# Performance work log

Hardware: AMD Instinct MI355X
Metric: run time of the kernel (lower is better)

## Reference

```python
import jax, jax.numpy as jnp
import numpy as np

B, L, D, H, DK, DV = 2, 2048, 512, 8, 64, 64
EPS = 1e-6


def setup_inputs() -> dict:
    key = jax.random.key(0)
    ks = jax.random.split(key, 19)
    n = lambda k, s: jax.random.normal(k, s, dtype=jnp.float32)
    inp = {
        "q_r": n(ks[0], (B, L, D)), "q_i": n(ks[1], (B, L, D)),
        "k_r": n(ks[2], (B, L, D)), "k_i": n(ks[3], (B, L, D)),
        "v_r": n(ks[4], (B, L, D)), "v_i": n(ks[5], (B, L, D)),
        "wq_r": n(ks[6], (D, H * DK)) * 0.02, "wq_i": n(ks[7], (D, H * DK)) * 0.02,
        "wk_r": n(ks[8], (D, H * DK)) * 0.02, "wk_i": n(ks[9], (D, H * DK)) * 0.02,
        "wv_r": n(ks[10], (D, H * DV)) * 0.02, "wv_i": n(ks[11], (D, H * DV)) * 0.02,
        "wo_r": n(ks[12], (H * DV, D)) * 0.02, "wo_i": n(ks[13], (H * DV, D)) * 0.02,
        "ln_wr": n(ks[14], (D,)), "ln_wi": n(ks[15], (D,)),
        "ln_br": n(ks[16], (D,)), "ln_bi": n(ks[17], (D,)),
        "mask": jax.random.randint(ks[18], (B, L, L), 0, 2).astype(jnp.int32),
    }
    return inp


def _clinear(xr, xi, wr, wi):
    # complex matmul (xr + i xi) @ (wr + i wi)
    return xr @ wr - xi @ wi, xi @ wr + xr @ wi


def _complex_layernorm(r, i, wr, wi, br, bi, eps=EPS):
    axes = (1, 2)  # normalize over all non-batch dims of [B, L, D]
    r = r - r.mean(axis=axes, keepdims=True)
    i = i - i.mean(axis=axes, keepdims=True)
    Crr = (r * r).mean(axis=axes, keepdims=True) + eps
    Cii = (i * i).mean(axis=axes, keepdims=True) + eps
    Cri = (r * i).mean(axis=axes, keepdims=True)
    s = jnp.sqrt(Crr * Cii - Cri * Cri)
    t = jnp.sqrt(Crr + Cii + 2.0 * s)
    inv_st = 1.0 / (s * t)
    Rrr = (Cii + s) * inv_st
    Rii = (Crr + s) * inv_st
    Rri = -Cri * inv_st
    nr = Rrr * r + Rri * i
    ni = Rii * i + Rri * r
    # affine: complex multiply by (wr + i wi), then add complex bias
    out_r = nr * wr - ni * wi + br
    out_i = nr * wi + ni * wr + bi
    return out_r, out_i


def reference(q_r, q_i, k_r, k_i, v_r, v_i,
              wq_r, wq_i, wk_r, wk_i, wv_r, wv_i, wo_r, wo_i,
              ln_wr, ln_wi, ln_br, ln_bi, mask):
    res_r, res_i = q_r, q_i
    qr, qi = _clinear(q_r, q_i, wq_r, wq_i)
    kr, ki = _clinear(k_r, k_i, wk_r, wk_i)
    vr, vi = _clinear(v_r, v_i, wv_r, wv_i)
    # [B, L, H*Dk] -> [B, H, L, Dk]
    tohead = lambda x, d: x.reshape(B, L, H, d).transpose(0, 2, 1, 3)
    qr, qi = tohead(qr, DK), tohead(qi, DK)
    kr, ki = tohead(kr, DK), tohead(ki, DK)
    vr, vi = tohead(vr, DV), tohead(vi, DV)
    temp = jnp.float32(DK) ** 0.5
    qr, qi = qr / temp, qi / temp
    # complex scores (q @ conj(k)^T): re + i*im
    sr = jnp.einsum('bhqd,bhkd->bhqk', qr, kr) + jnp.einsum('bhqd,bhkd->bhqk', qi, ki)
    si = jnp.einsum('bhqd,bhkd->bhqk', qi, kr) - jnp.einsum('bhqd,bhkd->bhqk', qr, ki)
    a = jnp.sqrt(sr * sr + si * si)  # abs of complex scores
    a = jnp.where(mask[:, None, :, :] == 0, jnp.float32(-1e9), a)
    attn = jax.nn.softmax(a, axis=-1)  # real-valued attention weights
    out_r = jnp.einsum('bhqk,bhkd->bhqd', attn, vr)
    out_i = jnp.einsum('bhqk,bhkd->bhqd', attn, vi)
    # [B, H, L, Dv] -> [B, L, H*Dv]
    out_r = out_r.transpose(0, 2, 1, 3).reshape(B, L, H * DV)
    out_i = out_i.transpose(0, 2, 1, 3).reshape(B, L, H * DV)
    out_r, out_i = _clinear(out_r, out_i, wo_r, wo_i)
    out_r = out_r + res_r
    out_i = out_i + res_i
    out_r, out_i = _complex_layernorm(out_r, out_i, ln_wr, ln_wi, ln_br, ln_bi)
    return out_r, out_i, attn
```

## Files before the change

### kernel.cpp

```cpp
#include <hip/hip_runtime.h>

typedef unsigned short u16;
typedef unsigned int u32;
typedef unsigned long long u64;


typedef __attribute__((ext_vector_type(8))) short bf16x8;
typedef __attribute__((ext_vector_type(4))) float f32x4;
typedef __attribute__((ext_vector_type(4))) u32 u32x4;

__device__ __forceinline__ u16 f2bf(float f) {
  u32 x = __float_as_uint(f);
  return (u16)((x + 0x7FFFu + ((x >> 16) & 1u)) >> 16);
}
__device__ __forceinline__ u32 pk2(float a, float b) {
  return (u32)f2bf(a) | ((u32)f2bf(b) << 16);
}
__device__ __forceinline__ bf16x8 negv(bf16x8 v) {
  u32x4 x = __builtin_bit_cast(u32x4, v);
  x ^= 0x80008000u;
  return __builtin_bit_cast(bf16x8, x);
}

__global__ __launch_bounds__(256) void prep(
    const float* __restrict__ qr, const float* __restrict__ qi,
    const float* __restrict__ kr, const float* __restrict__ ki,
    const float* __restrict__ vr, const float* __restrict__ vi,
    const float* __restrict__ wqr, const float* __restrict__ wqi,
    const float* __restrict__ wkr, const float* __restrict__ wki,
    const float* __restrict__ wvr, const float* __restrict__ wvi,
    const float* __restrict__ wor, const float* __restrict__ woi,
    const int* __restrict__ mask,
    u16* __restrict__ A, u16* __restrict__ Btb, u64* __restrict__ mb,
    float* __restrict__ stats) {
  __shared__ float tile[64][65];
  int bid = blockIdx.x;
  int t = threadIdx.x;
  if (bid < 32768) {
    int tid = bid * 256 + t;
    u64 bal = __ballot(mask[tid] != 0);
    if ((t & 63) == 0) mb[tid >> 6] = bal;
    return;
  }
  bid -= 32768;
  if (bid < 6144) {
    int z = bid >> 11;
    int bx = bid & 2047;
    const float* r  = (z == 0) ? qr : (z == 1) ? kr : vr;
    const float* im = (z == 0) ? qi : (z == 1) ? ki : vi;
    int c = bx * 256 + t;
    int m = c >> 7;
    int ck = (c & 127) * 8;
    const float* s = (ck < 512) ? (r + (size_t)m * 512 + ck)
                                : (im + (size_t)m * 512 + (ck - 512));
    float4 a = ((const float4*)s)[0];
    float4 b = ((const float4*)s)[1];
    uint4 o;
    o.x = pk2(a.x, a.y); o.y = pk2(a.z, a.w);
    o.z = pk2(b.x, b.y); o.w = pk2(b.z, b.w);
    ((uint4*)(A + (size_t)z * 4194304))[c] = o;
    return;
  }
  bid -= 6144;
  if (bid < 1024) {
    int z = bid >> 8;
    int bx = bid & 255;
    const float* wr = (z==0)?wqr:(z==1)?wkr:(z==2)?wvr:wor;
    const float* wi = (z==0)?wqi:(z==1)?wki:(z==2)?wvi:woi;
    u16* Bt = Btb + (size_t)z * 1048576;
    int n0 = (bx >> 4) * 64;
    int k0 = (bx & 15) * 64;
    bool nlow = (n0 < 512), klow = (k0 < 512);
    const float* src = nlow ? (klow ? wr : wi) : (klow ? wi : wr);
    float sgn = (nlow && !klow) ? -1.0f : 1.0f;
    int col0 = nlow ? n0 : n0 - 512;
    int kr0 = klow ? k0 : k0 - 512;
    {
      int rr = t >> 2, cc = (t & 3) * 16;
      const float4* s = (const float4*)(src + (size_t)(kr0 + rr) * 512 + col0 + cc);
#pragma unroll
      for (int j = 0; j < 4; ++j) {
        float4 v = s[j];
        tile[rr][cc + j*4 + 0] = v.x; tile[rr][cc + j*4 + 1] = v.y;
        tile[rr][cc + j*4 + 2] = v.z; tile[rr][cc + j*4 + 3] = v.w;
      }
    }
    __syncthreads();
    {
      int nn = t >> 2, kc = (t & 3) * 16;
      u32 w[8];
#pragma unroll
      for (int j = 0; j < 8; ++j)
        w[j] = pk2(sgn * tile[kc + 2*j][nn], sgn * tile[kc + 2*j + 1][nn]);
      uint4* d = (uint4*)(Bt + (size_t)(n0 + nn) * 1024 + k0 + kc);
      d[0] = make_uint4(w[0], w[1], w[2], w[3]);
      d[1] = make_uint4(w[4], w[5], w[6], w[7]);
    }
    return;
  }
  if (t < 16) stats[t] = 0.0f;
}

__global__ __launch_bounds__(256) void pack_vt(const u16* __restrict__ Cvm,
                                               u16* __restrict__ vt) {
  int z = blockIdx.y;
  int b = z >> 3, h = z & 7;
  int lt = blockIdx.x >> 1, ct = blockIdx.x & 1;
  int l0 = lt * 64, c0 = ct * 64;
  int n0 = (ct == 0) ? (h * 64) : (512 + h * 64);
  __shared__ u16 tile[64][80];
  int t = threadIdx.x;
  {
    int lr = t >> 2, cc = (t & 3) * 16;
    const uint4* s = (const uint4*)(Cvm + ((size_t)(b * 2048 + l0 + lr)) * 1024 + n0 + cc);
    uint4 v0 = s[0], v1 = s[1];
    *(uint4*)&tile[lr][cc] = v0;
    *(uint4*)&tile[lr][cc + 8] = v1;
  }
  __syncthreads();
  {
    int cr = t >> 2, lc = (t & 3) * 16;
    u32 w[8];
#pragma unroll
    for (int j = 0; j < 8; ++j)
      w[j] = (u32)tile[lc + 2*j][cr] | ((u32)tile[lc + 2*j + 1][cr] << 16);
    uint4* d = (uint4*)(vt + ((size_t)z * 128 + c0 + cr) * 2048 + l0 + lc);
    d[0] = make_uint4(w[0], w[1], w[2], w[3]);
    d[1] = make_uint4(w[4], w[5], w[6], w[7]);
  }
}

__device__ __forceinline__ void glds128(const u16* __restrict__ g, int ld,
                                        u16* lds, int t) {
  int lane = t & 63, w = t >> 6;
  int sub = lane >> 3;
  int cs = (lane & 7) ^ sub;
#pragma unroll
  for (int p = 0; p < 4; ++p) {
    int r = p * 32 + w * 8 + sub;
    const u16* ga = g + (size_t)r * ld + cs * 8;
    u16* la = lds + (size_t)(p * 32 + w * 8) * 64;
    __builtin_amdgcn_global_load_lds(
        (const __attribute__((address_space(1))) void*)ga,
        (__attribute__((address_space(3))) void*)la, 16, 0, 0);
  }
}
__device__ __forceinline__ void glds64(const u16* __restrict__ g, int ld,
                                       u16* lds, int t) {
  int lane = t & 63, w = t >> 6;
  int sub = lane >> 3;
  int cs = (lane & 7) ^ sub;
#pragma unroll
  for (int p = 0; p < 2; ++p) {
    int r = p * 32 + w * 8 + sub;
    const u16* ga = g + (size_t)r * ld + cs * 8;
    u16* la = lds + (size_t)(p * 32 + w * 8) * 64;
    __builtin_amdgcn_global_load_lds(
        (const __attribute__((address_space(1))) void*)ga,
        (__attribute__((address_space(3))) void*)la, 16, 0, 0);
  }
}

__global__ __launch_bounds__(256) void gemm_proj(const u16* __restrict__ Abase,
                                                 const u16* __restrict__ Btbase,
                                                 u16* __restrict__ Cbase) {
  __shared__ u16 lA[128 * 64], lB[128 * 64];
  int t = threadIdx.x, lane = t & 63, wid = t >> 6;
  int c15 = lane & 15, g = lane >> 4, l7 = lane & 7;
  int z = blockIdx.z;
  const u16* A  = Abase  + (size_t)z * 4194304;
  const u16* Bt = Btbase + (size_t)z * 1048576;
  u16* C = Cbase + (size_t)z * 4194304;
  int brow = blockIdx.y * 128, bcol = blockIdx.x * 128;
  float scale = (z == 0) ? 0.125f : 1.0f;
  int sw0 = ((g ^ l7) << 3), sw1 = (((4 | g) ^ l7) << 3);
  int wr0 = (wid >> 1) * 64 + c15, wc0 = (wid & 1) * 64 + c15;
  const u16 *pA0 = lA + wr0 * 64 + sw0, *pA1 = lA + wr0 * 64 + sw1;
  const u16 *pB0 = lB + wc0 * 64 + sw0, *pB1 = lB + wc0 * 64 + sw1;
  f32x4 zero = {0.f, 0.f, 0.f, 0.f};
  f32x4 acc[4][4];
#pragma unroll
  for (int mi = 0; mi < 4; ++mi)
#pragma unroll
    for (int ni = 0; ni < 4; ++ni) acc[mi][ni] = zero;
  for (int kt = 0; kt < 1024; kt += 64) {
    glds128(A + (size_t)brow * 1024 + kt, 1024, lA, t);
    glds128(Bt + (size_t)bcol * 1024 + kt, 1024, lB, t);
    __syncthreads();
#pragma unroll
    for (int ks = 0; ks < 2; ++ks) {
      const u16* pa = ks ? pA1 : pA0;
      const u16* pb = ks ? pB1 : pB0;
      bf16x8 fa[4], fb[4];
#pragma unroll
      for (int i2 = 0; i2 < 4; ++i2) {
        fa[i2] = *(const bf16x8*)(pa + i2 * 1024);
        fb[i2] = *(const bf16x8*)(pb + i2 * 1024);
      }
#pragma unroll
      for (int mi = 0; mi < 4; ++mi)
#pragma unroll
        for (int ni = 0; ni < 4; ++ni)
          acc[mi][ni] = __builtin_amdgcn_mfma_f32_16x16x32_bf16(
              fa[mi], fb[ni], acc[mi][ni], 0, 0, 0);
    }
    __syncthreads();
  }
  int wrb = (wid >> 1) * 64, wcb = (wid & 1) * 64;
  int rj = g * 4, cj = c15;
#pragma unroll
  for (int mi = 0; mi < 4; ++mi)
#pragma unroll
    for (int ni = 0; ni < 4; ++ni)
#pragma unroll
      for (int j = 0; j < 4; ++j)
        C[(size_t)(brow + wrb + mi * 16 + rj + j) * 1024 +
          (bcol + wcb + ni * 16 + cj)] = f2bf(acc[mi][ni][j] * scale);
}

__global__ __launch_bounds__(256, 3) void fused_p1(
    const u16* __restrict__ Cq, const u16* __restrict__ Ck,
    const u16* __restrict__ vt, const u64* __restrict__ mb,
    float* __restrict__ invbuf, u16* __restrict__ Ao) {
  __shared__ u16 lKr[64 * 64], lKi[64 * 64], lV[128 * 64], lP[64 * 64];
  int t = threadIdx.x, lane = t & 63, w = t >> 6;
  int c15 = lane & 15, g = lane >> 4, l7 = lane & 7;
  int f = blockIdx.x + (int)gridDim.x * blockIdx.y;
  int wk = (f & 7) * 64 + (f >> 3);
  int strip = wk & 31, z = wk >> 5;
  int b = z >> 3, h = z & 7;
  int q0 = strip * 64;
  int arow = w * 16 + c15;
  int rbase = w * 16 + (g << 2);

  const u16* Qrow = Cq + ((size_t)(b * 2048 + q0 + arow)) * 1024 + h * 64;
  bf16x8 q0r = *(const bf16x8*)(Qrow + g * 8);
  bf16x8 q1r = *(const bf16x8*)(Qrow + 32 + g * 8);
  bf16x8 q0i = *(const bf16x8*)(Qrow + 512 + g * 8);
  bf16x8 q1i = *(const bf16x8*)(Qrow + 544 + g * 8);
  bf16x8 nq0r = negv(q0r), nq1r = negv(q1r);

  int sw0 = ((g ^ l7) << 3), sw1 = (((4 | g) ^ l7) << 3);
  const u16 *pKr0 = lKr + c15 * 64 + sw0, *pKr1 = lKr + c15 * 64 + sw1;
  const u16 *pKi0 = lKi + c15 * 64 + sw0, *pKi1 = lKi + c15 * 64 + sw1;
  const u16 *pV0 = lV + c15 * 64 + sw0, *pV1 = lV + c15 * 64 + sw1;
  const u16 *pP0 = lP + arow * 64 + sw0, *pP1 = lP + arow * 64 + sw1;

  size_t mbase = ((size_t)(b * 2048 + q0 + rbase)) * 32;
  float s[4] = {0.f, 0.f, 0.f, 0.f};
  f32x4 zero = {0.f, 0.f, 0.f, 0.f};
  f32x4 o[8];
#pragma unroll
  for (int ni = 0; ni < 8; ++ni) o[ni] = zero;

  const u16* Kb = Ck + ((size_t)(b * 2048)) * 1024 + h * 64;
  const u16* Vb = vt + (size_t)z * 262144;

  for (int tl = 0; tl < 32; ++tl) {
    int l0 = tl * 64;
    if (tl) __syncthreads();
    glds64(Kb + (size_t)l0 * 1024, 1024, lKr, t);
    glds64(Kb + (size_t)l0 * 1024 + 512, 1024, lKi, t);
    glds128(Vb + l0, 2048, lV, t);
    __syncthreads();
    f32x4 sr[4], si[4];
#pragma unroll
    for (int ni = 0; ni < 4; ++ni) { sr[ni] = zero; si[ni] = zero; }
#pragma unroll
    for (int ni = 0; ni < 4; ++ni) {
      bf16x8 g0 = *(const bf16x8*)(pKr0 + ni * 1024);
      bf16x8 g1 = *(const bf16x8*)(pKi0 + ni * 1024);
      sr[ni] = __builtin_amdgcn_mfma_f32_16x16x32_bf16(q0r, g0, sr[ni], 0, 0, 0);
      sr[ni] = __builtin_amdgcn_mfma_f32_16x16x32_bf16(q0i, g1, sr[ni], 0, 0, 0);
      si[ni] = __builtin_amdgcn_mfma_f32_16x16x32_bf16(q0i, g0, si[ni], 0, 0, 0);
      si[ni] = __builtin_amdgcn_mfma_f32_16x16x32_bf16(nq0r, g1, si[ni], 0, 0, 0);
      bf16x8 h0 = *(const bf16x8*)(pKr1 + ni * 1024);
      bf16x8 h1 = *(const bf16x8*)(pKi1 + ni * 1024);
      sr[ni] = __builtin_amdgcn_mfma_f32_16x16x32_bf16(q1r, h0, sr[ni], 0, 0, 0);
      sr[ni] = __builtin_amdgcn_mfma_f32_16x16x32_bf16(q1i, h1, sr[ni], 0, 0, 0);
      si[ni] = __builtin_amdgcn_mfma_f32_16x16x32_bf16(q1i, h0, si[ni], 0, 0, 0);
      si[ni] = __builtin_amdgcn_mfma_f32_16x16x32_bf16(nq1r, h1, si[ni], 0, 0, 0);
    }
    u64 wm[4];
#pragma unroll
    for (int j = 0; j < 4; ++j) wm[j] = mb[mbase + (size_t)j * 32 + tl];
#pragma unroll
    for (int ni = 0; ni < 4; ++ni) {
      int cbit = ni * 16 + c15;
      int pchi = ni * 2 + (c15 >> 3);
#pragma unroll
      for (int j = 0; j < 4; ++j) {
        float n = sr[ni][j] * sr[ni][j] + si[ni][j] * si[ni][j];
        float p = __expf(__builtin_amdgcn_sqrtf(n));
        p = ((wm[j] >> cbit) & 1ull) ? p : 0.0f;
        s[j] += p;
        lP[(rbase + j) * 64 + ((pchi ^ (((g & 1) << 2) + j)) << 3) + l7] = f2bf(p);
      }
    }
    {
      bf16x8 fa0 = *(const bf16x8*)pP0;
      bf16x8 fa1 = *(const bf16x8*)pP1;
#pragma unroll
      for (int ni = 0; ni < 8; ++ni) {
        bf16x8 fb0 = *(const bf16x8*)(pV0 + ni * 1024);
        bf16x8 fb1 = *(const bf16x8*)(pV1 + ni * 1024);
        o[ni] = __builtin_amdgcn_mfma_f32_16x16x32_bf16(fa0, fb0, o[ni], 0, 0, 0);
        o[ni] = __builtin_amdgcn_mfma_f32_16x16x32_bf16(fa1, fb1, o[ni], 0, 0, 0);
      }
    }
  }
  float inv[4];
#pragma unroll
  for (int j = 0; j < 4; ++j) {
    float sj = s[j];
#pragma unroll
    for (int off = 1; off < 16; off <<= 1) sj += __shfl_xor(sj, off);
    inv[j] = 1.0f / sj;
  }
  if (c15 == 0) {
#pragma unroll
    for (int j = 0; j < 4; ++j)
      invbuf[z * 2048 + q0 + rbase + j] = inv[j];
  }
#pragma unroll
  for (int ni = 0; ni < 8; ++ni) {
    int c = ni * 16 + c15;
    int nout = (c < 64) ? (h * 64 + c) : (512 + h * 64 + (c - 64));
#pragma unroll
    for (int j = 0; j < 4; ++j)
      Ao[((size_t)(b * 2048 + q0 + rbase + j)) * 1024 + nout] =
          f2bf(o[ni][j] * inv[j]);
  }
}

__global__ __launch_bounds__(256, 3) void attn_p2(
    const u16* __restrict__ Cq, const u16* __restrict__ Ck,
    const u64* __restrict__ mb, const float* __restrict__ invbuf,
    float* __restrict__ attn) {
  __shared__ u16 lKr[64 * 64], lKi[64 * 64];
  int t = threadIdx.x, lane = t & 63, w = t >> 6;
  int c15 = lane & 15, g = lane >> 4, l7 = lane & 7;
  int f = blockIdx.x + (int)gridDim.x * blockIdx.y;
  int wk = (f & 7) * 256 + (f >> 3);
  int z = wk >> 7;
  int rem = wk & 127;
  int strip = rem >> 2, kc = rem & 3;
  int b = z >> 3, h = z & 7;
  int q0 = strip * 64;
  int arow = w * 16 + c15;
  int rbase = w * 16 + (g << 2);

  const u16* Qrow = Cq + ((size_t)(b * 2048 + q0 + arow)) * 1024 + h * 64;
  bf16x8 q0r = *(const bf16x8*)(Qrow + g * 8);
  bf16x8 q1r = *(const bf16x8*)(Qrow + 32 + g * 8);
  bf16x8 q0i = *(const bf16x8*)(Qrow + 512 + g * 8);
  bf16x8 q1i = *(const bf16x8*)(Qrow + 544 + g * 8);
  bf16x8 nq0r = negv(q0r), nq1r = negv(q1r);

  int sw0 = ((g ^ l7) << 3), sw1 = (((4 | g) ^ l7) << 3);
  const u16 *pKr0 = lKr + c15 * 64 + sw0, *pKr1 = lKr + c15 * 64 + sw1;
  const u16 *pKi0 = lKi + c15 * 64 + sw0, *pKi1 = lKi + c15 * 64 + sw1;

  size_t mbase = ((size_t)(b * 2048 + q0 + rbase)) * 32;
  float inv[4];
#pragma unroll
  for (int j = 0; j < 4; ++j) inv[j] = invbuf[z * 2048 + q0 + rbase + j];
  f32x4 zero = {0.f, 0.f, 0.f, 0.f};
  const u16* Kb = Ck + ((size_t)(b * 2048)) * 1024 + h * 64;
  float* arow_out = attn + ((size_t)z * 2048 + q0 + rbase) * 2048 + c15;

  for (int tt2 = 0; tt2 < 8; ++tt2) {
    int tl = kc * 8 + tt2;
    int l0 = tl * 64;
    if (tt2) __syncthreads();
    glds64(Kb + (size_t)l0 * 1024, 1024, lKr, t);
    glds64(Kb + (size_t)l0 * 1024 + 512, 1024, lKi, t);
    __syncthreads();
    f32x4 sr[4], si[4];
#pragma unroll
    for (int ni = 0; ni < 4; ++ni) { sr[ni] = zero; si[ni] = zero; }
#pragma unroll
    for (int ni = 0; ni < 4; ++ni) {
      bf16x8 g0 = *(const bf16x8*)(pKr0 + ni * 1024);
      bf16x8 g1 = *(const bf16x8*)(pKi0 + ni * 1024);
      sr[ni] = __builtin_amdgcn_mfma_f32_16x16x32_bf16(q0r, g0, sr[ni], 0, 0, 0);
      sr[ni] = __builtin_amdgcn_mfma_f32_16x16x32_bf16(q0i, g1, sr[ni], 0, 0, 0);
      si[ni] = __builtin_amdgcn_mfma_f32_16x16x32_bf16(q0i, g0, si[ni], 0, 0, 0);
      si[ni] = __builtin_amdgcn_mfma_f32_16x16x32_bf16(nq0r, g1, si[ni], 0, 0, 0);
      bf16x8 h0 = *(const bf16x8*)(pKr1 + ni * 1024);
      bf16x8 h1 = *(const bf16x8*)(pKi1 + ni * 1024);
      sr[ni] = __builtin_amdgcn_mfma_f32_16x16x32_bf16(q1r, h0, sr[ni], 0, 0, 0);
      sr[ni] = __builtin_amdgcn_mfma_f32_16x16x32_bf16(q1i, h1, sr[ni], 0, 0, 0);
      si[ni] = __builtin_amdgcn_mfma_f32_16x16x32_bf16(q1i, h0, si[ni], 0, 0, 0);
      si[ni] = __builtin_amdgcn_mfma_f32_16x16x32_bf16(nq1r, h1, si[ni], 0, 0, 0);
    }
    u64 wm[4];
#pragma unroll
    for (int j = 0; j < 4; ++j) wm[j] = mb[mbase + (size_t)j * 32 + tl];
    float* outp = arow_out + l0;
#pragma unroll
    for (int ni = 0; ni < 4; ++ni) {
      int cbit = ni * 16 + c15;
#pragma unroll
      for (int j = 0; j < 4; ++j) {
        float n = sr[ni][j] * sr[ni][j] + si[ni][j] * si[ni][j];
        float p = __expf(__builtin_amdgcn_sqrtf(n)) * inv[j];
        p = ((wm[j] >> cbit) & 1ull) ? p : 0.0f;
        outp[(size_t)j * 2048 + ni * 16] = p;
      }
    }
  }
}

__global__ __launch_bounds__(256) void gemm_oproj(
    const u16* __restrict__ A, const u16* __restrict__ Bt,
    const float* __restrict__ resR, const float* __restrict__ resI,
    float* __restrict__ outR, float* __restrict__ outI) {
  __shared__ u16 lA[128 * 64], lB[128 * 64];
  int t = threadIdx.x, lane = t & 63, wid = t >> 6;
  int c15 = lane & 15, g = lane >> 4, l7 = lane & 7;
  int brow = blockIdx.y * 128, bcol = blockIdx.x * 128;
  int sw0 = ((g ^ l7) << 3), sw1 = (((4 | g) ^ l7) << 3);
  int wr0 = (wid >> 1) * 64 + c15, wc0 = (wid & 1) * 64 + c15;
  const u16 *pA0 = lA + wr0 * 64 + sw0, *pA1 = lA + wr0 * 64 + sw1;
  const u16 *pB0 = lB + wc0 * 64 + sw0, *pB1 = lB + wc0 * 64 + sw1;
  f32x4 zero = {0.f, 0.f, 0.f, 0.f};
  f32x4 acc[4][4];
#pragma unroll
  for (int mi = 0; mi < 4; ++mi)
#pragma unroll
    for (int ni = 0; ni < 4; ++ni) acc[mi][ni] = zero;
  for (int kt = 0; kt < 1024; kt += 64) {
    glds128(A + (size_t)brow * 1024 + kt, 1024, lA, t);
    glds128(Bt + (size_t)bcol * 1024 + kt, 1024, lB, t);
    __syncthreads();
#pragma unroll
    for (int ks = 0; ks < 2; ++ks) {
      const u16* pa = ks ? pA1 : pA0;
      const u16* pb = ks ? pB1 : pB0;
      bf16x8 fa[4], fb[4];
#pragma unroll
      for (int i2 = 0; i2 < 4; ++i2) {
        fa[i2] = *(const bf16x8*)(pa + i2 * 1024);
        fb[i2] = *(const bf16x8*)(pb + i2 * 1024);
      }
#pragma unroll
      for (int mi = 0; mi < 4; ++mi)
#pragma unroll
        for (int ni = 0; ni < 4; ++ni)
          acc[mi][ni] = __builtin_amdgcn_mfma_f32_16x16x32_bf16(
              fa[mi], fb[ni], acc[mi][ni], 0, 0, 0);
    }
    __syncthreads();
  }
  int wrb = (wid >> 1) * 64, wcb = (wid & 1) * 64;
  int rj = g * 4, cj = c15;
#pragma unroll
  for (int mi = 0; mi < 4; ++mi)
#pragma unroll
    for (int ni = 0; ni < 4; ++ni)
#pragma unroll
      for (int j = 0; j < 4; ++j) {
        int row = brow + wrb + mi * 16 + rj + j;
        int col = bcol + wcb + ni * 16 + cj;
        float v = acc[mi][ni][j];
        if (col < 512)
          outR[(size_t)row * 512 + col] = v + resR[(size_t)row * 512 + col];
        else {
          int c2 = col - 512;
          outI[(size_t)row * 512 + c2] = v + resI[(size_t)row * 512 + c2];
        }
      }
}

__global__ __launch_bounds__(256) void ln_reduce(const float* __restrict__ outR,
                                                 const float* __restrict__ outI,
                                                 float* __restrict__ stats) {
  int b = blockIdx.y;
  int t = threadIdx.x;
  size_t base = (size_t)b * 1048576 + (size_t)blockIdx.x * 2048;
  float s0 = 0.f, s1 = 0.f, s2 = 0.f, s3 = 0.f, s4 = 0.f;
#pragma unroll
  for (int p = 0; p < 8; ++p) {
    size_t e = base + p * 256 + t;
    float r = outR[e], i = outI[e];
    s0 += r; s1 += i; s2 += r * r; s3 += i * i; s4 += r * i;
  }
#pragma unroll
  for (int off = 32; off; off >>= 1) {
    s0 += __shfl_xor(s0, off); s1 += __shfl_xor(s1, off);
    s2 += __shfl_xor(s2, off); s3 += __shfl_xor(s3, off);
    s4 += __shfl_xor(s4, off);
  }
  __shared__ float red[4][5];
  if ((t & 63) == 0) {
    int w = t >> 6;
    red[w][0] = s0; red[w][1] = s1; red[w][2] = s2; red[w][3] = s3; red[w][4] = s4;
  }
  __syncthreads();
  if (t == 0) {
    float a0 = red[0][0] + red[1][0] + red[2][0] + red[3][0];
    float a1 = red[0][1] + red[1][1] + red[2][1] + red[3][1];
    float a2 = red[0][2] + red[1][2] + red[2][2] + red[3][2];
    float a3 = red[0][3] + red[1][3] + red[2][3] + red[3][3];
    float a4 = red[0][4] + red[1][4] + red[2][4] + red[3][4];
    atomicAdd(&stats[b * 8 + 0], a0);
    atomicAdd(&stats[b * 8 + 1], a1);
    atomicAdd(&stats[b * 8 + 2], a2);
    atomicAdd(&stats[b * 8 + 3], a3);
    atomicAdd(&stats[b * 8 + 4], a4);
  }
}

__global__ __launch_bounds__(256) void ln_apply(
    float* __restrict__ outR, float* __restrict__ outI,
    const float* __restrict__ stats,
    const float* __restrict__ lnwr, const float* __restrict__ lnwi,
    const float* __restrict__ lnbr, const float* __restrict__ lnbi) {
  int b = blockIdx.y;
  const float* st = stats + b * 8;
  float iN = 1.0f / 1048576.0f;
  float mr = st[0] * iN, mi = st[1] * iN;
  float Crr = st[2] * iN - mr * mr + 1e-6f;
  float Cii = st[3] * iN - mi * mi + 1e-6f;
  float Cri = st[4] * iN - mr * mi;
  float s = sqrtf(fmaxf(Crr * Cii - Cri * Cri, 0.f));
  float tt = sqrtf(Crr + Cii + 2.f * s);
  float inv = 1.0f / (s * tt);
  float Rrr = (Cii + s) * inv, Rii = (Crr + s) * inv, Rri = -Cri * inv;
  size_t e = ((size_t)blockIdx.x * 256 + threadIdx.x) * 4;
  size_t idx = (size_t)b * 1048576 + e;
  int d = (int)(e & 511);
  float4 r4 = *(float4*)(outR + idx);
  float4 i4 = *(float4*)(outI + idx);
  float4 wr = *(const float4*)(lnwr + d);
  float4 wi = *(const float4*)(lnwi + d);
  float4 br = *(const float4*)(lnbr + d);
  float4 bi = *(const float4*)(lnbi + d);
  float4 orr, oii;
#pragma unroll
  for (int j = 0; j < 4; ++j) {
    float r = ((&r4.x)[j]) - mr;
    float i = ((&i4.x)[j]) - mi;
    float nr = Rrr * r + Rri * i;
    float ni = Rii * i + Rri * r;
    (&orr.x)[j] = nr * (&wr.x)[j] - ni * (&wi.x)[j] + (&br.x)[j];
    (&oii.x)[j] = nr * (&wi.x)[j] + ni * (&wr.x)[j] + (&bi.x)[j];
  }
  *(float4*)(outR + idx) = orr;
  *(float4*)(outI + idx) = oii;
}

extern "C" void kernel_launch(void* const* d_in, const int* in_sizes, int n_in,
                              void* d_out, int out_size, void* d_ws, size_t ws_size,
                              hipStream_t stream) {
  const float* q_r = (const float*)d_in[0];
  const float* q_i = (const float*)d_in[1];
  const float* k_r = (const float*)d_in[2];
  const float* k_i = (const float*)d_in[3];
  const float* v_r = (const float*)d_in[4];
  const float* v_i = (const float*)d_in[5];
  const float* wq_r = (const float*)d_in[6];
  const float* wq_i = (const float*)d_in[7];
  const float* wk_r = (const float*)d_in[8];
  const float* wk_i = (const float*)d_in[9];
  const float* wv_r = (const float*)d_in[10];
  const float* wv_i = (const float*)d_in[11];
  const float* wo_r = (const float*)d_in[12];
  const float* wo_i = (const float*)d_in[13];
  const float* ln_wr = (const float*)d_in[14];
  const float* ln_wi = (const float*)d_in[15];
  const float* ln_br = (const float*)d_in[16];
  const float* ln_bi = (const float*)d_in[17];
  const int* mask = (const int*)d_in[18];

  float* outR = (float*)d_out;
  float* outI = outR + 2097152;
  float* attn = outR + 4194304;

  char* ws = (char*)d_ws;
  u16* Aq = (u16*)ws;
  u16* Bt = (u16*)(ws + 25165824);
  u16* Cq = (u16*)(ws + 33554432);
  u16* Ck = Cq + 4194304;
  u16* Cv = Cq + 8388608;
  u16* vt = Aq;
  u16* Ao = (u16*)(ws + 58720256);
  u64* mb = (u64*)(ws + 67108864);
  float* stats = (float*)(ws + 69206016);
  float* invbuf = (float*)(ws + 69207040);

  prep<<<dim3(32768 + 6144 + 1024 + 1), 256, 0, stream>>>(
      q_r, q_i, k_r, k_i, v_r, v_i, wq_r, wq_i, wk_r, wk_i, wv_r, wv_i,
      wo_r, wo_i, mask, Aq, Bt, mb, stats);
  gemm_proj<<<dim3(8, 32, 3), 256, 0, stream>>>(Aq, Bt, Cq);
  pack_vt<<<dim3(64, 16), 256, 0, stream>>>(Cv, vt);
  fused_p1<<<dim3(32, 16), 256, 0, stream>>>(Cq, Ck, vt, mb, invbuf, Ao);
  attn_p2<<<dim3(128, 16), 256, 0, stream>>>(Cq, Ck, mb, invbuf, attn);
  gemm_oproj<<<dim3(8, 32), 256, 0, stream>>>(Ao, Bt + 3145728, q_r, q_i, outR, outI);
  ln_reduce<<<dim3(512, 2), 256, 0, stream>>>(outR, outI, stats);
  ln_apply<<<dim3(1024, 2), 256, 0, stream>>>(outR, outI, stats, ln_wr, ln_wi,
                                              ln_br, ln_bi);
}
```

Baseline: 338.1 us.

## Halve attention block threads, give each wave two 16-row query tiles

The fused attention and attn-probability kernels now launch 128 threads (2 waves) per 64-row strip instead of 4. Each wave handles 32 query rows, so every K and V fragment read from LDS feeds two tiles' worth of MFMAs. LDS load helpers are rewritten to fill the same tiles with fewer threads. This cuts LDS read traffic per MFMA but doubles register use and halves waves per block, which lowers latency hiding and occupancy.

```diff
diff --git a/kernel.cpp b/kernel.cpp
--- a/kernel.cpp
+++ b/kernel.cpp
@@ -145,16 +145,31 @@
         (__attribute__((address_space(3))) void*)la, 16, 0, 0);
   }
 }
-__device__ __forceinline__ void glds64(const u16* __restrict__ g, int ld,
-                                       u16* lds, int t) {
+__device__ __forceinline__ void glds64h(const u16* __restrict__ g, int ld,
+                                        u16* lds, int t) {
   int lane = t & 63, w = t >> 6;
   int sub = lane >> 3;
   int cs = (lane & 7) ^ sub;
 #pragma unroll
-  for (int p = 0; p < 2; ++p) {
-    int r = p * 32 + w * 8 + sub;
+  for (int p = 0; p < 4; ++p) {
+    int r = p * 16 + w * 8 + sub;
     const u16* ga = g + (size_t)r * ld + cs * 8;
-    u16* la = lds + (size_t)(p * 32 + w * 8) * 64;
+    u16* la = lds + (size_t)(p * 16 + w * 8) * 64;
+    __builtin_amdgcn_global_load_lds(
+        (const __attribute__((address_space(1))) void*)ga,
+        (__attribute__((address_space(3))) void*)la, 16, 0, 0);
+  }
+}
+__device__ __forceinline__ void glds128h(const u16* __restrict__ g, int ld,
+                                         u16* lds, int t) {
+  int lane = t & 63, w = t >> 6;
+  int sub = lane >> 3;
+  int cs = (lane & 7) ^ sub;
+#pragma unroll
+  for (int p = 0; p < 8; ++p) {
+    int r = p * 16 + w * 8 + sub;
+    const u16* ga = g + (size_t)r * ld + cs * 8;
+    u16* la = lds + (size_t)(p * 16 + w * 8) * 64;
     __builtin_amdgcn_global_load_lds(
         (const __attribute__((address_space(1))) void*)ga,
         (__attribute__((address_space(3))) void*)la, 16, 0, 0);
@@ -218,7 +233,7 @@
           (bcol + wcb + ni * 16 + cj)] = f2bf(acc[mi][ni][j] * scale);
 }
 
-__global__ __launch_bounds__(256, 3) void fused_p1(
+__global__ __launch_bounds__(128) void fused_p1(
     const u16* __restrict__ Cq, const u16* __restrict__ Ck,
     const u16* __restrict__ vt, const u64* __restrict__ mb,
     float* __restrict__ invbuf, u16* __restrict__ Ao) {
@@ -230,28 +245,38 @@
   int strip = wk & 31, z = wk >> 5;
   int b = z >> 3, h = z & 7;
   int q0 = strip * 64;
-  int arow = w * 16 + c15;
-  int rbase = w * 16 + (g << 2);
-
-  const u16* Qrow = Cq + ((size_t)(b * 2048 + q0 + arow)) * 1024 + h * 64;
-  bf16x8 q0r = *(const bf16x8*)(Qrow + g * 8);
-  bf16x8 q1r = *(const bf16x8*)(Qrow + 32 + g * 8);
-  bf16x8 q0i = *(const bf16x8*)(Qrow + 512 + g * 8);
-  bf16x8 q1i = *(const bf16x8*)(Qrow + 544 + g * 8);
-  bf16x8 nq0r = negv(q0r), nq1r = negv(q1r);
+  int arow = w * 32 + c15;
+  int rbase = w * 32 + (g << 2);
+
+  bf16x8 q0r[2], q1r[2], q0i[2], q1i[2], nq0r[2], nq1r[2];
+#pragma unroll
+  for (int rq = 0; rq < 2; ++rq) {
+    const u16* Qrow =
+        Cq + ((size_t)(b * 2048 + q0 + arow + rq * 16)) * 1024 + h * 64;
+    q0r[rq] = *(const bf16x8*)(Qrow + g * 8);
+    q1r[rq] = *(const bf16x8*)(Qrow + 32 + g * 8);
+    q0i[rq] = *(const bf16x8*)(Qrow + 512 + g * 8);
+    q1i[rq] = *(const bf16x8*)(Qrow + 544 + g * 8);
+    nq0r[rq] = negv(q0r[rq]);
+    nq1r[rq] = negv(q1r[rq]);
+  }
 
   int sw0 = ((g ^ l7) << 3), sw1 = (((4 | g) ^ l7) << 3);
   const u16 *pKr0 = lKr + c15 * 64 + sw0, *pKr1 = lKr + c15 * 64 + sw1;
   const u16 *pKi0 = lKi + c15 * 64 + sw0, *pKi1 = lKi + c15 * 64 + sw1;
   const u16 *pV0 = lV + c15 * 64 + sw0, *pV1 = lV + c15 * 64 + sw1;
-  const u16 *pP0 = lP + arow * 64 + sw0, *pP1 = lP + arow * 64 + sw1;
+  const u16 *pPa0 = lP + arow * 64 + sw0, *pPa1 = lP + arow * 64 + sw1;
+  const u16 *pPb0 = lP + (arow + 16) * 64 + sw0;
+  const u16 *pPb1 = lP + (arow + 16) * 64 + sw1;
 
   size_t mbase = ((size_t)(b * 2048 + q0 + rbase)) * 32;
-  float s[4] = {0.f, 0.f, 0.f, 0.f};
+  float s[2][4] = {{0.f, 0.f, 0.f, 0.f}, {0.f, 0.f, 0.f, 0.f}};
   f32x4 zero = {0.f, 0.f, 0.f, 0.f};
-  f32x4 o[8];
-#pragma unroll
-  for (int ni = 0; ni < 8; ++ni) o[ni] = zero;
+  f32x4 o[2][8];
+#pragma unroll
+  for (int rq = 0; rq < 2; ++rq)
+#pragma unroll
+    for (int ni = 0; ni < 8; ++ni) o[rq][ni] = zero;
 
   const u16* Kb = Ck + ((size_t)(b * 2048)) * 1024 + h * 64;
   const u16* Vb = vt + (size_t)z * 262144;
@@ -259,81 +284,98 @@
   for (int tl = 0; tl < 32; ++tl) {
     int l0 = tl * 64;
     if (tl) __syncthreads();
-    glds64(Kb + (size_t)l0 * 1024, 1024, lKr, t);
-    glds64(Kb + (size_t)l0 * 1024 + 512, 1024, lKi, t);
-    glds128(Vb + l0, 2048, lV, t);
+    glds64h(Kb + (size_t)l0 * 1024, 1024, lKr, t);
+    glds64h(Kb + (size_t)l0 * 1024 + 512, 1024, lKi, t);
+    glds128h(Vb + l0, 2048, lV, t);
     __syncthreads();
-    f32x4 sr[4], si[4];
-#pragma unroll
-    for (int ni = 0; ni < 4; ++ni) { sr[ni] = zero; si[ni] = zero; }
+    f32x4 sr[2][4], si[2][4];
+#pragma unroll
+    for (int rq = 0; rq < 2; ++rq)
+#pragma unroll
+      for (int ni = 0; ni < 4; ++ni) { sr[rq][ni] = zero; si[rq][ni] = zero; }
 #pragma unroll
     for (int ni = 0; ni < 4; ++ni) {
       bf16x8 g0 = *(const bf16x8*)(pKr0 + ni * 1024);
       bf16x8 g1 = *(const bf16x8*)(pKi0 + ni * 1024);
-      sr[ni] = __builtin_amdgcn_mfma_f32_16x16x32_bf16(q0r, g0, sr[ni], 0, 0, 0);
-      sr[ni] = __builtin_amdgcn_mfma_f32_16x16x32_bf16(q0i, g1, sr[ni], 0, 0, 0);
-      si[ni] = __builtin_amdgcn_mfma_f32_16x16x32_bf16(q0i, g0, si[ni], 0, 0, 0);
-      si[ni] = __builtin_amdgcn_mfma_f32_16x16x32_bf16(nq0r, g1, si[ni], 0, 0, 0);
       bf16x8 h0 = *(const bf16x8*)(pKr1 + ni * 1024);
       bf16x8 h1 = *(const bf16x8*)(pKi1 + ni * 1024);
-      sr[ni] = __builtin_amdgcn_mfma_f32_16x16x32_bf16(q1r, h0, sr[ni], 0, 0, 0);
-      sr[ni] = __builtin_amdgcn_mfma_f32_16x16x32_bf16(q1i, h1, sr[ni], 0, 0, 0);
-      si[ni] = __builtin_amdgcn_mfma_f32_16x16x32_bf16(q1i, h0, si[ni], 0, 0, 0);
-      si[ni] = __builtin_amdgcn_mfma_f32_16x16x32_bf16(nq1r, h1, si[ni], 0, 0, 0);
-    }
-    u64 wm[4];
-#pragma unroll
-    for (int j = 0; j < 4; ++j) wm[j] = mb[mbase + (size_t)j * 32 + tl];
-#pragma unroll
-    for (int ni = 0; ni < 4; ++ni) {
-      int cbit = ni * 16 + c15;
-      int pchi = ni * 2 + (c15 >> 3);
-#pragma unroll
-      for (int j = 0; j < 4; ++j) {
-        float n = sr[ni][j] * sr[ni][j] + si[ni][j] * si[ni][j];
-        float p = __expf(__builtin_amdgcn_sqrtf(n));
-        p = ((wm[j] >> cbit) & 1ull) ? p : 0.0f;
-        s[j] += p;
-        lP[(rbase + j) * 64 + ((pchi ^ (((g & 1) << 2) + j)) << 3) + l7] = f2bf(p);
+#pragma unroll
+      for (int rq = 0; rq < 2; ++rq) {
+        sr[rq][ni] = __builtin_amdgcn_mfma_f32_16x16x32_bf16(q0r[rq], g0, sr[rq][ni], 0, 0, 0);
+        sr[rq][ni] = __builtin_amdgcn_mfma_f32_16x16x32_bf16(q0i[rq], g1, sr[rq][ni], 0, 0, 0);
+        si[rq][ni] = __builtin_amdgcn_mfma_f32_16x16x32_bf16(q0i[rq], g0, si[rq][ni], 0, 0, 0);
+        si[rq][ni] = __builtin_amdgcn_mfma_f32_16x16x32_bf16(nq0r[rq], g1, si[rq][ni], 0, 0, 0);
+        sr[rq][ni] = __builtin_amdgcn_mfma_f32_16x16x32_bf16(q1r[rq], h0, sr[rq][ni], 0, 0, 0);
+        sr[rq][ni] = __builtin_amdgcn_mfma_f32_16x16x32_bf16(q1i[rq], h1, sr[rq][ni], 0, 0, 0);
+        si[rq][ni] = __builtin_amdgcn_mfma_f32_16x16x32_bf16(q1i[rq], h0, si[rq][ni], 0, 0, 0);
+        si[rq][ni] = __builtin_amdgcn_mfma_f32_16x16x32_bf16(nq1r[rq], h1, si[rq][ni], 0, 0, 0);
+      }
+    }
+#pragma unroll
+    for (int rq = 0; rq < 2; ++rq) {
+      u64 wm[4];
+#pragma unroll
+      for (int j = 0; j < 4; ++j)
+        wm[j] = mb[mbase + (size_t)rq * 512 + (size_t)j * 32 + tl];
+#pragma unroll
+      for (int ni = 0; ni < 4; ++ni) {
+        int cbit = ni * 16 + c15;
+        int pchi = ni * 2 + (c15 >> 3);
+#pragma unroll
+        for (int j = 0; j < 4; ++j) {
+          float n = sr[rq][ni][j] * sr[rq][ni][j] + si[rq][ni][j] * si[rq][ni][j];
+          float p = __expf(__builtin_amdgcn_sqrtf(n));
+          p = ((wm[j] >> cbit) & 1ull) ? p : 0.0f;
+          s[rq][j] += p;
+          lP[(rbase + rq * 16 + j) * 64 +
+             ((pchi ^ (((g & 1) << 2) + j)) << 3) + l7] = f2bf(p);
+        }
       }
     }
     {
-      bf16x8 fa0 = *(const bf16x8*)pP0;
-      bf16x8 fa1 = *(const bf16x8*)pP1;
+      bf16x8 fa0a = *(const bf16x8*)pPa0;
+      bf16x8 fa1a = *(const bf16x8*)pPa1;
+      bf16x8 fa0b = *(const bf16x8*)pPb0;
+      bf16x8 fa1b = *(const bf16x8*)pPb1;
 #pragma unroll
       for (int ni = 0; ni < 8; ++ni) {
         bf16x8 fb0 = *(const bf16x8*)(pV0 + ni * 1024);
         bf16x8 fb1 = *(const bf16x8*)(pV1 + ni * 1024);
-        o[ni] = __builtin_amdgcn_mfma_f32_16x16x32_bf16(fa0, fb0, o[ni], 0, 0, 0);
-        o[ni] = __builtin_amdgcn_mfma_f32_16x16x32_bf16(fa1, fb1, o[ni], 0, 0, 0);
-      }
-    }
-  }
-  float inv[4];
-#pragma unroll
-  for (int j = 0; j < 4; ++j) {
-    float sj = s[j];
-#pragma unroll
-    for (int off = 1; off < 16; off <<= 1) sj += __shfl_xor(sj, off);
-    inv[j] = 1.0f / sj;
-  }
-  if (c15 == 0) {
-#pragma unroll
-    for (int j = 0; j < 4; ++j)
-      invbuf[z * 2048 + q0 + rbase + j] = inv[j];
-  }
-#pragma unroll
-  for (int ni = 0; ni < 8; ++ni) {
-    int c = ni * 16 + c15;
-    int nout = (c < 64) ? (h * 64 + c) : (512 + h * 64 + (c - 64));
-#pragma unroll
-    for (int j = 0; j < 4; ++j)
-      Ao[((size_t)(b * 2048 + q0 + rbase + j)) * 1024 + nout] =
-          f2bf(o[ni][j] * inv[j]);
-  }
-}
-
-__global__ __launch_bounds__(256, 3) void attn_p2(
+        o[0][ni] = __builtin_amdgcn_mfma_f32_16x16x32_bf16(fa0a, fb0, o[0][ni], 0, 0, 0);
+        o[0][ni] = __builtin_amdgcn_mfma_f32_16x16x32_bf16(fa1a, fb1, o[0][ni], 0, 0, 0);
+        o[1][ni] = __builtin_amdgcn_mfma_f32_16x16x32_bf16(fa0b, fb0, o[1][ni], 0, 0, 0);
+        o[1][ni] = __builtin_amdgcn_mfma_f32_16x16x32_bf16(fa1b, fb1, o[1][ni], 0, 0, 0);
+      }
+    }
+  }
+#pragma unroll
+  for (int rq = 0; rq < 2; ++rq) {
+    float inv[4];
+#pragma unroll
+    for (int j = 0; j < 4; ++j) {
+      float sj = s[rq][j];
+#pragma unroll
+      for (int off = 1; off < 16; off <<= 1) sj += __shfl_xor(sj, off);
+      inv[j] = 1.0f / sj;
+    }
+    if (c15 == 0) {
+#pragma unroll
+      for (int j = 0; j < 4; ++j)
+        invbuf[z * 2048 + q0 + rbase + rq * 16 + j] = inv[j];
+    }
+#pragma unroll
+    for (int ni = 0; ni < 8; ++ni) {
+      int c = ni * 16 + c15;
+      int nout = (c < 64) ? (h * 64 + c) : (512 + h * 64 + (c - 64));
+#pragma unroll
+      for (int j = 0; j < 4; ++j)
+        Ao[((size_t)(b * 2048 + q0 + rbase + rq * 16 + j)) * 1024 + nout] =
+            f2bf(o[rq][ni][j] * inv[j]);
+    }
+  }
+}
+
+__global__ __launch_bounds__(128) void attn_p2(
     const u16* __restrict__ Cq, const u16* __restrict__ Ck,
     const u64* __restrict__ mb, const float* __restrict__ invbuf,
     float* __restrict__ attn) {
@@ -347,66 +389,85 @@
   int strip = rem >> 2, kc = rem & 3;
   int b = z >> 3, h = z & 7;
   int q0 = strip * 64;
-  int arow = w * 16 + c15;
-  int rbase = w * 16 + (g << 2);
-
-  const u16* Qrow = Cq + ((size_t)(b * 2048 + q0 + arow)) * 1024 + h * 64;
-  bf16x8 q0r = *(const bf16x8*)(Qrow + g * 8);
-  bf16x8 q1r = *(const bf16x8*)(Qrow + 32 + g * 8);
-  bf16x8 q0i = *(const bf16x8*)(Qrow + 512 + g * 8);
-  bf16x8 q1i = *(const bf16x8*)(Qrow + 544 + g * 8);
-  bf16x8 nq0r = negv(q0r), nq1r = negv(q1r);
+  int arow = w * 32 + c15;
+  int rbase = w * 32 + (g << 2);
+
+  bf16x8 q0r[2], q1r[2], q0i[2], q1i[2], nq0r[2], nq1r[2];
+#pragma unroll
+  for (int rq = 0; rq < 2; ++rq) {
+    const u16* Qrow =
+        Cq + ((size_t)(b * 2048 + q0 + arow + rq * 16)) * 1024 + h * 64;
+    q0r[rq] = *(const bf16x8*)(Qrow + g * 8);
+    q1r[rq] = *(const bf16x8*)(Qrow + 32 + g * 8);
+    q0i[rq] = *(const bf16x8*)(Qrow + 512 + g * 8);
+    q1i[rq] = *(const bf16x8*)(Qrow + 544 + g * 8);
+    nq0r[rq] = negv(q0r[rq]);
+    nq1r[rq] = negv(q1r[rq]);
+  }
 
   int sw0 = ((g ^ l7) << 3), sw1 = (((4 | g) ^ l7) << 3);
   const u16 *pKr0 = lKr + c15 * 64 + sw0, *pKr1 = lKr + c15 * 64 + sw1;
   const u16 *pKi0 = lKi + c15 * 64 + sw0, *pKi1 = lKi + c15 * 64 + sw1;
 
   size_t mbase = ((size_t)(b * 2048 + q0 + rbase)) * 32;
-  float inv[4];
-#pragma unroll
-  for (int j = 0; j < 4; ++j) inv[j] = invbuf[z * 2048 + q0 + rbase + j];
+  float inv[2][4];
+#pragma unroll
+  for (int rq = 0; rq < 2; ++rq)
+#pragma unroll
+    for (int j = 0; j < 4; ++j)
+      inv[rq][j] = invbuf[z * 2048 + q0 + rbase + rq * 16 + j];
   f32x4 zero = {0.f, 0.f, 0.f, 0.f};
   const u16* Kb = Ck + ((size_t)(b * 2048)) * 1024 + h * 64;
-  float* arow_out = attn + ((size_t)z * 2048 + q0 + rbase) * 2048 + c15;
+  float* out0 = attn + ((size_t)z * 2048 + q0 + rbase) * 2048 + c15;
+  float* out1 = out0 + (size_t)16 * 2048;
 
   for (int tt2 = 0; tt2 < 8; ++tt2) {
     int tl = kc * 8 + tt2;
     int l0 = tl * 64;
     if (tt2) __syncthreads();
-    glds64(Kb + (size_t)l0 * 1024, 1024, lKr, t);
-    glds64(Kb + (size_t)l0 * 1024 + 512, 1024, lKi, t);
+    glds64h(Kb + (size_t)l0 * 1024, 1024, lKr, t);
+    glds64h(Kb + (size_t)l0 * 1024 + 512, 1024, lKi, t);
     __syncthreads();
-    f32x4 sr[4], si[4];
-#pragma unroll
-    for (int ni = 0; ni < 4; ++ni) { sr[ni] = zero; si[ni] = zero; }
+    f32x4 sr[2][4], si[2][4];
+#pragma unroll
+    for (int rq = 0; rq < 2; ++rq)
+#pragma unroll
+      for (int ni = 0; ni < 4; ++ni) { sr[rq][ni] = zero; si[rq][ni] = zero; }
 #pragma unroll
     for (int ni = 0; ni < 4; ++ni) {
       bf16x8 g0 = *(const bf16x8*)(pKr0 + ni * 1024);
       bf16x8 g1 = *(const bf16x8*)(pKi0 + ni * 1024);
-      sr[ni] = __builtin_amdgcn_mfma_f32_16x16x32_bf16(q0r, g0, sr[ni], 0, 0, 0);
-      sr[ni] = __builtin_amdgcn_mfma_f32_16x16x32_bf16(q0i, g1, sr[ni], 0, 0, 0);
-      si[ni] = __builtin_amdgcn_mfma_f32_16x16x32_bf16(q0i, g0, si[ni], 0, 0, 0);
-      si[ni] = __builtin_amdgcn_mfma_f32_16x16x32_bf16(nq0r, g1, si[ni], 0, 0, 0);
       bf16x8 h0 = *(const bf16x8*)(pKr1 + ni * 1024);
       bf16x8 h1 = *(const bf16x8*)(pKi1 + ni * 1024);
-      sr[ni] = __builtin_amdgcn_mfma_f32_16x16x32_bf16(q1r, h0, sr[ni], 0, 0, 0);
-      sr[ni] = __builtin_amdgcn_mfma_f32_16x16x32_bf16(q1i, h1, sr[ni], 0, 0, 0);
-      si[ni] = __builtin_amdgcn_mfma_f32_16x16x32_bf16(q1i, h0, si[ni], 0, 0, 0);
-      si[ni] = __builtin_amdgcn_mfma_f32_16x16x32_bf16(nq1r, h1, si[ni], 0, 0, 0);
-    }
-    u64 wm[4];
-#pragma unroll
-    for (int j = 0; j < 4; ++j) wm[j] = mb[mbase + (size_t)j * 32 + tl];
-    float* outp = arow_out + l0;
-#pragma unroll
-    for (int ni = 0; ni < 4; ++ni) {
-      int cbit = ni * 16 + c15;
-#pragma unroll
-      for (int j = 0; j < 4; ++j) {
-        float n = sr[ni][j] * sr[ni][j] + si[ni][j] * si[ni][j];
-        float p = __expf(__builtin_amdgcn_sqrtf(n)) * inv[j];
-        p = ((wm[j] >> cbit) & 1ull) ? p : 0.0f;
-        outp[(size_t)j * 2048 + ni * 16] = p;
+#pragma unroll
+      for (int rq = 0; rq < 2; ++rq) {
+        sr[rq][ni] = __builtin_amdgcn_mfma_f32_16x16x32_bf16(q0r[rq], g0, sr[rq][ni], 0, 0, 0);
+        sr[rq][ni] = __builtin_amdgcn_mfma_f32_16x16x32_bf16(q0i[rq], g1, sr[rq][ni], 0, 0, 0);
+        si[rq][ni] = __builtin_amdgcn_mfma_f32_16x16x32_bf16(q0i[rq], g0, si[rq][ni], 0, 0, 0);
+        si[rq][ni] = __builtin_amdgcn_mfma_f32_16x16x32_bf16(nq0r[rq], g1, si[rq][ni], 0, 0, 0);
+        sr[rq][ni] = __builtin_amdgcn_mfma_f32_16x16x32_bf16(q1r[rq], h0, sr[rq][ni], 0, 0, 0);
+        sr[rq][ni] = __builtin_amdgcn_mfma_f32_16x16x32_bf16(q1i[rq], h1, sr[rq][ni], 0, 0, 0);
+        si[rq][ni] = __builtin_amdgcn_mfma_f32_16x16x32_bf16(q1i[rq], h0, si[rq][ni], 0, 0, 0);
+        si[rq][ni] = __builtin_amdgcn_mfma_f32_16x16x32_bf16(nq1r[rq], h1, si[rq][ni], 0, 0, 0);
+      }
+    }
+#pragma unroll
+    for (int rq = 0; rq < 2; ++rq) {
+      u64 wm[4];
+#pragma unroll
+      for (int j = 0; j < 4; ++j)
+        wm[j] = mb[mbase + (size_t)rq * 512 + (size_t)j * 32 + tl];
+      float* outp = (rq ? out1 : out0) + l0;
+#pragma unroll
+      for (int ni = 0; ni < 4; ++ni) {
+        int cbit = ni * 16 + c15;
+#pragma unroll
+        for (int j = 0; j < 4; ++j) {
+          float n = sr[rq][ni][j] * sr[rq][ni][j] + si[rq][ni][j] * si[rq][ni][j];
+          float p = __expf(__builtin_amdgcn_sqrtf(n)) * inv[rq][j];
+          p = ((wm[j] >> cbit) & 1ull) ? p : 0.0f;
+          outp[(size_t)j * 2048 + ni * 16] = p;
+        }
       }
     }
   }
@@ -595,8 +656,8 @@
       wo_r, wo_i, mask, Aq, Bt, mb, stats);
   gemm_proj<<<dim3(8, 32, 3), 256, 0, stream>>>(Aq, Bt, Cq);
   pack_vt<<<dim3(64, 16), 256, 0, stream>>>(Cv, vt);
-  fused_p1<<<dim3(32, 16), 256, 0, stream>>>(Cq, Ck, vt, mb, invbuf, Ao);
-  attn_p2<<<dim3(128, 16), 256, 0, stream>>>(Cq, Ck, mb, invbuf, attn);
+  fused_p1<<<dim3(32, 16), 128, 0, stream>>>(Cq, Ck, vt, mb, invbuf, Ao);
+  attn_p2<<<dim3(128, 16), 128, 0, stream>>>(Cq, Ck, mb, invbuf, attn);
   gemm_oproj<<<dim3(8, 32), 256, 0, stream>>>(Ao, Bt + 3145728, q_r, q_i, outR, outI);
   ln_reduce<<<dim3(512, 2), 256, 0, stream>>>(outR, outI, stats);
   ln_apply<<<dim3(1024, 2), 256, 0, stream>>>(outR, outI, stats, ln_wr, ln_wi,
```

Measured after the change: 359.3 us. +6.3%, slower.
